# Performance work log

Hardware: AMD Instinct MI355X
Metric: run time of the kernel (lower is better)

Reference implementation:

```python
import jax, jax.numpy as jnp
import numpy as np

# Conv config (matches init_kwargs)
STRIDE = (1, 1)
PADDING = ((1, 1), (1, 1))
B, CIN, COUT, H, W = 16, 128, 256, 56, 56
KH, KW = 3, 3


def _conv(x, w):
    # NCHW input, OIHW kernel, zeros padding mode
    return jax.lax.conv_general_dilated(
        x, w, window_strides=STRIDE, padding=PADDING,
        dimension_numbers=("NCHW", "OIHW", "NCHW"))


def setup_inputs() -> dict:
    key = jax.random.key(0)
    ks = jax.random.split(key, 6)
    x = jax.random.normal(ks[0], (B, CIN, H, W), dtype=jnp.float32)
    # quantized weight: integer-valued floats (output of module.Q.quantize)
    weight = jnp.round(jax.random.normal(ks[1], (COUT, CIN, KH, KW), dtype=jnp.float32) * 4.0)
    act_s = jnp.asarray(0.0625, dtype=jnp.float32)   # exp2(log_act_s)
    act_q = jnp.asarray(16.0, dtype=jnp.float32)     # exp2(log_act_q)
    azp = jnp.asarray(-4.0, dtype=jnp.float32)       # rounded act zero point (scaled by guard_a)
    wzp = jnp.round(jax.random.normal(ks[2], (COUT,), dtype=jnp.float32) * 2.0)
    fp_scale = (jax.random.uniform(ks[3], (1, COUT, 1, 1), dtype=jnp.float32) + 0.5) * 1e-3
    # bias_full has spatial extent [1, COUT, H_out, W_out]
    bias = jax.random.normal(ks[4], (1, COUT, H, W), dtype=jnp.float32) * 0.1
    guard_a = jnp.asarray(2.0, dtype=jnp.float32)    # 2**act_guard_bit
    guard_w = jnp.asarray(2.0, dtype=jnp.float32)    # 2**weight_guard_bit
    return {"x": x, "weight": weight, "act_s": act_s, "act_q": act_q,
            "azp": azp, "wzp": wzp, "fp_scale": fp_scale, "bias": bias,
            "guard_a": guard_a, "guard_w": guard_w}


def reference(x, weight, act_s, act_q, azp, wzp, fp_scale, bias, guard_a, guard_w):
    # 1) Activation quantization: clamp to quant range then round to integer grid.
    zp = azp * act_s / guard_a
    xq = jnp.clip(x, zp, zp + act_q - act_s)
    xq = guard_a * jnp.round((xq - zp) / act_s)
    # 2) Main integer conv with quantized weights.
    c1 = _conv(xq, weight)
    # 3) Ones-kernel conv: output is identical across all COUT channels,
    #    so compute once as channel-sum followed by a single-channel box conv.
    s = jnp.sum(xq, axis=1, keepdims=True)  # [B, 1, H, W]
    ones_k = jnp.ones((1, 1) + weight.shape[2:], dtype=x.dtype)
    c2 = _conv(s, ones_k)  # [B, 1, H_out, W_out], broadcasts over channels
    # 4) Affine dequant + spatially-varying bias epilogue.
    out = guard_w * c1 + wzp[None, :, None, None] * c2
    return out * fp_scale + bias
```

## Files before the change

kernel.cpp:

```cpp
#include <hip/hip_runtime.h>

#define B_    16
#define CIN_  128
#define COUT_ 256
#define H_    56
#define W_    56
#define YP    58
#define XP    64

typedef int   i32x4 __attribute__((ext_vector_type(4)));

#define BH_SZ 16640

__device__ __forceinline__ void gload16(const void* g, void* l) {
    __builtin_amdgcn_global_load_lds(
        (const __attribute__((address_space(1))) unsigned int*)g,
        (__attribute__((address_space(3))) unsigned int*)l,
        16, 0, 0);
}

__global__ __launch_bounds__(256) void k_prep(
    const float* __restrict__ x, const float* __restrict__ w,
    const float* __restrict__ p_act_s, const float* __restrict__ p_act_q,
    const float* __restrict__ p_azp,  const float* __restrict__ p_guard_a,
    signed char* __restrict__ xqU, signed char* __restrict__ wt,
    float* __restrict__ s_pad, float* __restrict__ Wsum)
{
    int t = threadIdx.x;
    int blk = blockIdx.x;

    if (blk < 928) {
        int b = blk / YP, y = blk - b * YP;
        __shared__ signed char shq[W_ * 144];
        signed char* orow = xqU + (size_t)blk * XP * CIN_;

        if (y == 0 || y == YP - 1) {
            i32x4 pv = {(int)0x80808080, (int)0x80808080,
                        (int)0x80808080, (int)0x80808080};
            *(i32x4*)(orow + t * 32)      = pv;
            *(i32x4*)(orow + t * 32 + 16) = pv;
            if (t < XP) s_pad[(size_t)blk * XP + t] = 0.0f;
            return;
        }
        int h = y - 1;
        float act_s = p_act_s[0], act_q = p_act_q[0];
        float azp = p_azp[0], ga = p_guard_a[0];
        float zp = azp * act_s / ga;
        float hi = zp + act_q - act_s;
        float inv_s = 1.0f / act_s;

        for (int i = 0; i < 28; ++i) {
            int e = i * 256 + t;
            int cin = e / 56;
            int ww = e - cin * 56;
            float v = x[(((size_t)b * CIN_ + cin) * H_ + h) * W_ + ww];
            v = fminf(fmaxf(v, zp), hi);
            float r = rintf((v - zp) * inv_s);
            float uq = rintf(ga * r * 0.5f) - 128.0f;
            shq[ww * 144 + cin] = (signed char)(int)uq;
        }
        __syncthreads();
        #pragma unroll
        for (int i = 0; i < 2; ++i) {
            int T = i * 256 + t;
            int xx = T >> 3;
            int c16 = T & 7;
            union { i32x4 v; signed char c[16]; } u;
            if (xx >= 1 && xx <= W_) {
                u.v = *(const i32x4*)(shq + (xx - 1) * 144 + c16 * 16);
            } else {
                u.v = (i32x4){(int)0x80808080, (int)0x80808080,
                              (int)0x80808080, (int)0x80808080};
            }
            *(i32x4*)(orow + (size_t)xx * CIN_ + c16 * 16) = u.v;
            int sum = 0;
            #pragma unroll
            for (int j = 0; j < 16; ++j) sum += (int)u.c[j];
            sum += __shfl_xor(sum, 1);
            sum += __shfl_xor(sum, 2);
            sum += __shfl_xor(sum, 4);
            if (c16 == 0)
                s_pad[(size_t)blk * XP + xx] = (float)(2 * sum + 32768);
        }
        return;
    }

    if (blk < 1216) {
        int o = ((blk - 928) * 256 + t) * 4;
        int tile = o >> 13;
        int m    = (o >> 6) & 127;
        int kk   = o & 63;
        int cb = tile & 1, cc = (tile >> 1) & 1, g = tile >> 2;
        int cout = cb * 128 + m;
        int cin0 = cc * 64 + kk;
        int dy = g / 3, dx = g - dy * 3;
        union { int v; signed char c[4]; } pk;
        #pragma unroll
        for (int j = 0; j < 4; ++j) {
            float v = w[(size_t)cout * 1152 + (cin0 + j) * 9 + dy * 3 + dx];
            pk.c[j] = (signed char)(int)v;
        }
        *(int*)(wt + o) = pk.v;
        return;
    }

    {
        int bw = blk - 1216;
        int cout = bw * 16 + (t >> 4);
        int part = t & 15;
        const float* base = w + (size_t)cout * 1152 + part * 72;
        float s = 0.f;
        for (int j = 0; j < 72; ++j) s += base[j];
        s += __shfl_xor(s, 1);
        s += __shfl_xor(s, 2);
        s += __shfl_xor(s, 4);
        s += __shfl_xor(s, 8);
        if (part == 0) Wsum[cout] = s;
        return;
    }
}

__global__ __launch_bounds__(256, 2) void k_gemm(
    const signed char* __restrict__ xqU,
    const signed char* __restrict__ wt,
    const float* __restrict__ s_pad,
    const float* __restrict__ Wsum,
    const float* __restrict__ wzp,
    const float* __restrict__ fps,
    const float* __restrict__ bias,
    const float* __restrict__ p_gw,
    float* __restrict__ out)
{
    __shared__ __align__(16) signed char Bh[2][BH_SZ];
    __shared__ float c2s[2 * 56];

    int tid = threadIdx.x;
    int wv = tid >> 6, lane = tid & 63;
    int xl = lane & 15, q = lane >> 4;
    int p = blockIdx.x, cb = blockIdx.y;
    int b = p / 28, hp = p - b * 28;
    int h = hp * 2;
    int wm0 = (wv >> 1) * 64;
    int row = wv & 1;

    if (tid < 112) {
        int rr = tid / 56, wp = tid - rr * 56;
        const float* sp = s_pad + ((size_t)(b * YP + h + rr)) * XP + wp;
        float a = 0.f;
        #pragma unroll
        for (int dy = 0; dy < 3; ++dy)
            #pragma unroll
            for (int dx = 0; dx < 3; ++dx)
                a += sp[dy * XP + dx];
        c2s[tid] = a;
    }

    const signed char* xb = xqU + (size_t)(b * YP + h) * XP * CIN_;

    #define STAGE_B(buf_, cc_)                                              \
        {                                                                   \
            signed char* dstb = Bh[buf_];                                   \
            _Pragma("unroll")                                               \
            for (int r_ = 0; r_ < 4; ++r_) {                                \
                int T_ = r_ * 256 + tid;                                    \
                int p_ = T_ & 3;                                            \
                int x_ = (T_ >> 2) & 63;                                    \
                int yy_ = T_ >> 8;                                          \
                int q_ = p_ ^ ((x_ >> 1) & 3);                              \
                gload16(xb + (size_t)(yy_ * XP + x_) * CIN_ + (cc_) * 64 + q_ * 16, \
                        dstb + (r_ * 256 + wv * 64) * 16);                  \
            }                                                               \
        }

    STAGE_B(0, 0)
    __syncthreads();

    i32x4 acc[4][4];
    #pragma unroll
    for (int mi = 0; mi < 4; ++mi)
        #pragma unroll
        for (int ni = 0; ni < 4; ++ni)
            acc[mi][ni] = (i32x4){0, 0, 0, 0};

    int aoff = (wm0 + xl) * 64 + q * 16;

    #pragma unroll
    for (int cc = 0; cc < 2; ++cc) {
        const signed char* Bb = Bh[cc];
        #pragma unroll
        for (int g = 0; g < 9; ++g) {
            if (cc == 0 && g == 0) STAGE_B(1, 1)
            int dy = g / 3, dx = g - dy * 3;
            const signed char* wtile =
                wt + (size_t)(((g * 2 + cc) * 2) + cb) * 8192;
            int slot = q ^ (((xl + dx) >> 1) & 3);
            int boff = (row + dy) * 4096 + (xl + dx) * 64 + slot * 16;
            i32x4 af[4], bf[4];
            #pragma unroll
            for (int mi = 0; mi < 4; ++mi)
                af[mi] = *(const i32x4*)(wtile + aoff + mi * 1024);
            #pragma unroll
            for (int ni = 0; ni < 4; ++ni)
                bf[ni] = *(const i32x4*)(Bb + boff + ni * 1024);
            #pragma unroll
            for (int mi = 0; mi < 4; ++mi)
                #pragma unroll
                for (int ni = 0; ni < 4; ++ni)
                    acc[mi][ni] = __builtin_amdgcn_mfma_i32_16x16x64_i8(
                        af[mi], bf[ni], acc[mi][ni], 0, 0, 0);
        }
        if (cc == 0) __syncthreads();
    }

    int hrow = h + row;
    float gw = p_gw[0];
    float c2v[4]; int wp4[4];
    #pragma unroll
    for (int ni = 0; ni < 4; ++ni) {
        int wp = ni * 16 + xl;
        wp4[ni] = wp;
        c2v[ni] = (wp < W_) ? c2s[row * 56 + wp] : 0.0f;
    }
    #pragma unroll
    for (int mi = 0; mi < 4; ++mi) {
        #pragma unroll
        for (int r = 0; r < 4; ++r) {
            int cout = cb * 128 + wm0 + mi * 16 + q * 4 + r;
            float wz = wzp[cout], fs = fps[cout], ws = Wsum[cout];
            const float* brow = bias + ((size_t)cout * H_ + hrow) * W_;
            float* orow = out + (((size_t)b * COUT_ + cout) * H_ + hrow) * W_;
            #pragma unroll
            for (int ni = 0; ni < 4; ++ni) {
                int wp = wp4[ni];
                if (wp < W_) {
                    float c1 = 2.0f * (float)acc[mi][ni][r] + 256.0f * ws;
                    float v = gw * c1 + wz * c2v[ni];
                    orow[wp] = v * fs + brow[wp];
                }
            }
        }
    }
}

extern "C" void kernel_launch(void* const* d_in, const int* in_sizes, int n_in,
                              void* d_out, int out_size, void* d_ws, size_t ws_size,
                              hipStream_t stream)
{
    const float* x     = (const float*)d_in[0];
    const float* wht   = (const float*)d_in[1];
    const float* act_s = (const float*)d_in[2];
    const float* act_q = (const float*)d_in[3];
    const float* azp   = (const float*)d_in[4];
    const float* wzp   = (const float*)d_in[5];
    const float* fps   = (const float*)d_in[6];
    const float* bias  = (const float*)d_in[7];
    const float* ga    = (const float*)d_in[8];
    const float* gw    = (const float*)d_in[9];
    float* out = (float*)d_out;

    char* ws = (char*)d_ws;
    signed char* xqU  = (signed char*)(ws);
    signed char* wt   = (signed char*)(ws + 7602176);
    float*       spad = (float*)(ws + 7602176 + 294912);
    float*       Wsum = (float*)(ws + 7602176 + 294912 + 237568);

    k_prep<<<dim3(1232), dim3(256), 0, stream>>>(
        x, wht, act_s, act_q, azp, ga, xqU, wt, spad, Wsum);
    k_gemm<<<dim3(448, 2), dim3(256), 0, stream>>>(
        xqU, wt, spad, Wsum, wzp, fps, bias, gw, out);
}
```

Measured before the change: 151.4 us.

## Stage GEMM epilogue through shared memory for vectorized coalesced stores; raise occupancy

```diff
diff --git a/kernel.cpp b/kernel.cpp
--- a/kernel.cpp
+++ b/kernel.cpp
@@ -9,8 +9,10 @@
 #define XP    64
 
 typedef int   i32x4 __attribute__((ext_vector_type(4)));
+typedef float f32x4 __attribute__((ext_vector_type(4)));
 
 #define BH_SZ 16640
+#define EP_STRIDE 68
 
 __device__ __forceinline__ void gload16(const void* g, void* l) {
     __builtin_amdgcn_global_load_lds(
@@ -120,7 +122,7 @@
     }
 }
 
-__global__ __launch_bounds__(256, 2) void k_gemm(
+__global__ __launch_bounds__(256, 3) void k_gemm(
     const signed char* __restrict__ xqU,
     const signed char* __restrict__ wt,
     const float* __restrict__ s_pad,
@@ -131,7 +133,10 @@
     const float* __restrict__ p_gw,
     float* __restrict__ out)
 {
-    __shared__ __align__(16) signed char Bh[2][BH_SZ];
+    __shared__ union {
+        signed char bh[2][BH_SZ];
+        float       ep[128 * EP_STRIDE];
+    } smem;
     __shared__ float c2s[2 * 56];
 
     int tid = threadIdx.x;
@@ -159,7 +164,7 @@
 
     #define STAGE_B(buf_, cc_)                                              \
         {                                                                   \
-            signed char* dstb = Bh[buf_];                                   \
+            signed char* dstb = smem.bh[buf_];                              \
             _Pragma("unroll")                                               \
             for (int r_ = 0; r_ < 4; ++r_) {                                \
                 int T_ = r_ * 256 + tid;                                    \
@@ -186,7 +191,7 @@
 
     #pragma unroll
     for (int cc = 0; cc < 2; ++cc) {
-        const signed char* Bb = Bh[cc];
+        const signed char* Bb = smem.bh[cc];
         #pragma unroll
         for (int g = 0; g < 9; ++g) {
             if (cc == 0 && g == 0) STAGE_B(1, 1)
@@ -212,33 +217,50 @@
         if (cc == 0) __syncthreads();
     }
 
-    int hrow = h + row;
+    __syncthreads();
+
     float gw = p_gw[0];
-    float c2v[4]; int wp4[4];
+    int cout_l = tid & 127;
+    int half   = tid >> 7;
+    int cout_g = cb * 128 + cout_l;
+    float fs = fps[cout_g];
+    float A  = gw * fs;
+    float K0 = 256.0f * gw * Wsum[cout_g] * fs;
+    float B0 = wzp[cout_g] * fs;
+
     #pragma unroll
-    for (int ni = 0; ni < 4; ++ni) {
-        int wp = ni * 16 + xl;
-        wp4[ni] = wp;
-        c2v[ni] = (wp < W_) ? c2s[row * 56 + wp] : 0.0f;
-    }
-    #pragma unroll
-    for (int mi = 0; mi < 4; ++mi) {
-        #pragma unroll
-        for (int r = 0; r < 4; ++r) {
-            int cout = cb * 128 + wm0 + mi * 16 + q * 4 + r;
-            float wz = wzp[cout], fs = fps[cout], ws = Wsum[cout];
-            const float* brow = bias + ((size_t)cout * H_ + hrow) * W_;
-            float* orow = out + (((size_t)b * COUT_ + cout) * H_ + hrow) * W_;
-            #pragma unroll
-            for (int ni = 0; ni < 4; ++ni) {
-                int wp = wp4[ni];
-                if (wp < W_) {
-                    float c1 = 2.0f * (float)acc[mi][ni][r] + 256.0f * ws;
-                    float v = gw * c1 + wz * c2v[ni];
-                    orow[wp] = v * fs + brow[wp];
-                }
+    for (int r2 = 0; r2 < 2; ++r2) {
+        if (row == r2) {
+            #pragma unroll
+            for (int mi = 0; mi < 4; ++mi)
+                #pragma unroll
+                for (int ni = 0; ni < 4; ++ni)
+                    #pragma unroll
+                    for (int r = 0; r < 4; ++r)
+                        smem.ep[(wm0 + mi * 16 + q * 4 + r) * EP_STRIDE +
+                                ni * 16 + xl] = 2.0f * (float)acc[mi][ni][r];
+        }
+        __syncthreads();
+        {
+            int hrow = h + r2;
+            const float* brow = bias + ((size_t)cout_g * H_ + hrow) * W_;
+            float* orow = out + (((size_t)b * COUT_ + cout_g) * H_ + hrow) * W_;
+            const float* eprow = smem.ep + cout_l * EP_STRIDE;
+            const float* c2row = c2s + r2 * 56;
+            #pragma unroll
+            for (int j = 0; j < 7; ++j) {
+                int w4 = (half * 7 + j) * 4;
+                f32x4 e = *(const f32x4*)(eprow + w4);
+                f32x4 bi = *(const f32x4*)(brow + w4);
+                f32x4 c2v = *(const f32x4*)(c2row + w4);
+                f32x4 v;
+                #pragma unroll
+                for (int kq = 0; kq < 4; ++kq)
+                    v[kq] = A * e[kq] + K0 + B0 * c2v[kq] + bi[kq];
+                *(f32x4*)(orow + w4) = v;
             }
         }
+        if (r2 == 0) __syncthreads();
     }
 }
 
```

Measured after the change: 153.7 us. About the same (+1.5%).
